# Kernel optimization log

Measured on AMD Instinct MI355X. Metric: run time of the kernel, lower is better.

## Reference

```python
import jax, jax.numpy as jnp
import numpy as np

N = 4096      # nodes (= attention seq_len)
D = 256       # dim_h
H = 4         # num_heads
HD = D // H   # head dim
E = 131072    # edges (avg degree 32)


def _ln(x, g, b, eps=1e-5):
    mu = jnp.mean(x, -1, keepdims=True)
    var = jnp.var(x, -1, keepdims=True)
    return (x - mu) * jax.lax.rsqrt(var + eps) * g + b


def setup_inputs() -> dict:
    key = jax.random.key(0)
    ks = jax.random.split(key, 10)
    s = 0.02
    nrm = lambda k, shape: jax.random.normal(k, shape, jnp.float32) * s
    return dict(
        x=jax.random.normal(ks[0], (N, D), jnp.float32),
        edge_index=jax.random.randint(ks[1], (2, E), 0, N, dtype=jnp.int32),
        W_gcn=nrm(ks[2], (D, D)), b_gcn=jnp.zeros((D,), jnp.float32),
        w_qkv=nrm(ks[3], (D, 3 * D)), b_qkv=jnp.zeros((3 * D,), jnp.float32),
        w_out=nrm(ks[4], (D, D)), b_out=jnp.zeros((D,), jnp.float32),
        g1l=jnp.ones((D,), jnp.float32), beta1l=jnp.zeros((D,), jnp.float32),
        g1a=jnp.ones((D,), jnp.float32), beta1a=jnp.zeros((D,), jnp.float32),
        W1=nrm(ks[5], (D, 2 * D)), bf1=jnp.zeros((2 * D,), jnp.float32),
        W2=nrm(ks[6], (2 * D, D)), bf2=jnp.zeros((D,), jnp.float32),
        g2=jnp.ones((D,), jnp.float32), beta2=jnp.zeros((D,), jnp.float32),
    )


def reference(x, edge_index, W_gcn, b_gcn, w_qkv, b_qkv, w_out, b_out,
              g1l, beta1l, g1a, beta1a, W1, bf1, W2, bf2, g2, beta2):
    n = x.shape[0]
    # --- GCNConv: sym-normalized aggregation with self loops ---
    loop = jnp.arange(n, dtype=edge_index.dtype)
    src = jnp.concatenate([edge_index[0], loop])
    dst = jnp.concatenate([edge_index[1], loop])
    deg = jax.ops.segment_sum(jnp.ones_like(src, x.dtype), dst, num_segments=n)
    dinv = jax.lax.rsqrt(deg)  # deg >= 1 thanks to self loops
    h = x @ W_gcn                                  # [N, D]
    msg = h[src] * (dinv[src] * dinv[dst])[:, None]  # gather + edge norm
    x_local = jax.ops.segment_sum(msg, dst, num_segments=n) + b_gcn
    x = _ln(x + x_local, g1l, beta1l)
    # --- Multi-head self-attention over all nodes (one sequence) ---
    qkv = x @ w_qkv + b_qkv
    q, k, v = jnp.split(qkv, 3, axis=-1)
    q = q.reshape(n, H, HD)
    k = k.reshape(n, H, HD)
    v = v.reshape(n, H, HD)
    scale = 1.0 / (HD ** 0.5)
    scores = jnp.einsum('nhd,mhd->hnm', q, k) * scale   # [H, N, N]
    attn = jax.nn.softmax(scores, axis=-1)
    x_attn = jnp.einsum('hnm,mhd->nhd', attn, v).reshape(n, D) @ w_out + b_out
    x = _ln(x + x_attn, g1a, beta1a)
    # --- FFN (D -> 2D -> D, ReLU) ---
    x_ffn = jax.nn.relu(x @ W1 + bf1) @ W2 + bf2
    return _ln(x + x_ffn, g2, beta2)
```

## Files before the change

kernel.cpp:

```cpp
#include <hip/hip_runtime.h>

typedef unsigned short u16;
typedef __bf16 bf16x8 __attribute__((ext_vector_type(8)));
typedef float f32x4 __attribute__((ext_vector_type(4)));

__device__ __forceinline__ u16 f2u(float f) {
    unsigned u = __builtin_bit_cast(unsigned, f);
    return (u16)((u + 0x7FFFu + ((u >> 16) & 1u)) >> 16);
}

__device__ __forceinline__ float u2f(u16 h) {
    return __builtin_bit_cast(float, (unsigned)h << 16);
}

__device__ __forceinline__ void glds16(const u16* g, u16* l) {
    __builtin_amdgcn_global_load_lds((const __attribute__((address_space(1))) unsigned int*)g,
                                     (__attribute__((address_space(3))) unsigned int*)l, 16, 0, 0);
}


__global__ __launch_bounds__(256) void prep_k(
    const float* __restrict__ w0, const float* __restrict__ w1, const float* __restrict__ w2,
    const float* __restrict__ w3, const float* __restrict__ w4, const float* __restrict__ x,
    u16* __restrict__ o0, u16* __restrict__ o1, u16* __restrict__ o2,
    u16* __restrict__ o3, u16* __restrict__ o4, u16* __restrict__ xo,
    int* __restrict__ cnt, int xblocks, int nn) {
    int b = blockIdx.x, t = threadIdx.x;
    if (b < 144) {
        const float* in; u16* out; int R, C, tb;
        if (b < 16)       { in = w0; out = o0; R = 256; C = 256; tb = b; }
        else if (b < 64)  { in = w1; out = o1; R = 256; C = 768; tb = b - 16; }
        else if (b < 80)  { in = w2; out = o2; R = 256; C = 256; tb = b - 64; }
        else if (b < 112) { in = w3; out = o3; R = 256; C = 512; tb = b - 80; }
        else              { in = w4; out = o4; R = 512; C = 256; tb = b - 112; }
        int tcols = C >> 6;
        int tr = tb / tcols, tc = tb - tr * tcols;
        __shared__ float T[64][65];
        int i0 = t >> 6, j = t & 63;
#pragma unroll
        for (int p = 0; p < 16; p++) {
            int r = p * 4 + i0;
            T[r][j] = in[(long)(tr * 64 + r) * C + tc * 64 + j];
        }
        __syncthreads();
#pragma unroll
        for (int p = 0; p < 16; p++) {
            int c = p * 4 + i0;
            out[(long)(tc * 64 + c) * R + tr * 64 + j] = f2u(T[j][c]);
        }
    } else if (b < 144 + xblocks) {
        long base = (long)(b - 144) * 4096;
#pragma unroll
        for (int p = 0; p < 4; p++) {
            long idx = base + p * 1024 + t * 4;
            float4 v = *(const float4*)&x[idx];
            unsigned lo = (unsigned)f2u(v.x) | ((unsigned)f2u(v.y) << 16);
            unsigned hi = (unsigned)f2u(v.z) | ((unsigned)f2u(v.w) << 16);
            *(uint2*)&xo[idx] = uint2{lo, hi};
        }
    } else {
        int i = (b - 144 - xblocks) * 256 + t;
        if (i < nn) cnt[i] = 0;
    }
}

__global__ void count_k(const int* __restrict__ ei, int E, int* __restrict__ cnt) {
    int e = blockIdx.x * 256 + threadIdx.x;
    if (e < E) atomicAdd(&cnt[ei[E + e]], 1);
}

__global__ __launch_bounds__(256) void scan_k(const int* __restrict__ cnt, int* __restrict__ offs,
                                              int* __restrict__ cur, float* __restrict__ dinv) {
    __shared__ int sums[256];
    int t = threadIdx.x;
    int base = t * 16;
    int loc[16]; int s = 0;
#pragma unroll
    for (int i = 0; i < 16; i++) { loc[i] = s; s += cnt[base + i]; }
    sums[t] = s;
    __syncthreads();
    for (int off = 1; off < 256; off <<= 1) {
        int v = (t >= off) ? sums[t - off] : 0;
        __syncthreads();
        sums[t] += v;
        __syncthreads();
    }
    int ex = (t == 0) ? 0 : sums[t - 1];
#pragma unroll
    for (int i = 0; i < 16; i++) {
        int o = ex + loc[i];
        offs[base + i] = o; cur[base + i] = o;
        dinv[base + i] = rsqrtf((float)(cnt[base + i] + 1));
    }
}

__global__ void scatter_k(const int* __restrict__ ei, int E, int* __restrict__ cur, int* __restrict__ srcs) {
    int e = blockIdx.x * 256 + threadIdx.x;
    if (e < E) {
        int s = ei[e], d = ei[E + e];
        int p = atomicAdd(&cur[d], 1);
        srcs[p] = s;
    }
}


__device__ __forceinline__ void block_ln_stats(float v, float& mu, float& rstd) {
    float s1 = v, s2 = v * v;
#pragma unroll
    for (int m = 1; m < 64; m <<= 1) { s1 += __shfl_xor(s1, m, 64); s2 += __shfl_xor(s2, m, 64); }
    __shared__ float r1[4], r2[4];
    int lane = threadIdx.x & 63, w = threadIdx.x >> 6;
    if (lane == 0) { r1[w] = s1; r2[w] = s2; }
    __syncthreads();
    s1 = r1[0] + r1[1] + r1[2] + r1[3];
    s2 = r2[0] + r2[1] + r2[2] + r2[3];
    mu = s1 * (1.0f / 256.0f);
    float var = s2 * (1.0f / 256.0f) - mu * mu;
    rstd = rsqrtf(var + 1e-5f);
}

__global__ __launch_bounds__(256) void ln_k(const float* __restrict__ a, const float* __restrict__ b,
                                            const float* __restrict__ g, const float* __restrict__ be,
                                            float* __restrict__ out, u16* __restrict__ outbf) {
    int n = blockIdx.x, d = threadIdx.x;
    long i = (long)n * 256 + d;
    float v = a[i] + b[i];
    float mu, rs;
    block_ln_stats(v, mu, rs);
    float y = (v - mu) * rs * g[d] + be[d];
    out[i] = y;
    if (outbf) outbf[i] = f2u(y);
}


__global__ __launch_bounds__(256) void gcn_agg_ln_k(
    const u16* __restrict__ h, const float* __restrict__ x,
    const int* __restrict__ srcs, const int* __restrict__ offs, const int* __restrict__ cnt,
    const float* __restrict__ dinv, const float* __restrict__ bg,
    const float* __restrict__ g, const float* __restrict__ be,
    float* __restrict__ x1, u16* __restrict__ x1bf) {
    int n = blockIdx.x, d = threadIdx.x;
    int c = cnt[n], st = offs[n];
    float dn = dinv[n];
    float agg = u2f(h[(long)n * 256 + d]) * dn;
    int e = 0;
    for (; e + 4 <= c; e += 4) {
        int s0 = srcs[st + e], s1 = srcs[st + e + 1], s2 = srcs[st + e + 2], s3 = srcs[st + e + 3];
        float a0 = u2f(h[(long)s0 * 256 + d]) * dinv[s0];
        float a1 = u2f(h[(long)s1 * 256 + d]) * dinv[s1];
        float a2 = u2f(h[(long)s2 * 256 + d]) * dinv[s2];
        float a3 = u2f(h[(long)s3 * 256 + d]) * dinv[s3];
        agg += (a0 + a1) + (a2 + a3);
    }
    for (; e < c; e++) {
        int s = srcs[st + e];
        agg += u2f(h[(long)s * 256 + d]) * dinv[s];
    }
    float v = x[(long)n * 256 + d] + dn * agg + bg[d];
    float mu, rs;
    block_ln_stats(v, mu, rs);
    float y = (v - mu) * rs * g[d] + be[d];
    x1[(long)n * 256 + d] = y;
    x1bf[(long)n * 256 + d] = f2u(y);
}


template <int EPI>
__global__ __launch_bounds__(256) void gemm_k(
    const u16* __restrict__ A, const u16* __restrict__ Bt,
    const float* __restrict__ bias, void* __restrict__ outp,
    int M, int N, int K) {
    __shared__ __align__(16) u16 As[64 * 256];
    __shared__ __align__(16) u16 Bs[64 * 256];
    int tid = threadIdx.x;
    int lane = tid & 63, w = tid >> 6;
    int l15 = lane & 15, quad = lane >> 4, l7 = l15 & 7;
    int m0 = blockIdx.x * 64, n0 = blockIdx.y * 64;
    int wm = (w >> 1) * 32, wn = (w & 1) * 32;
    f32x4 acc[2][2];
#pragma unroll
    for (int i = 0; i < 2; i++)
#pragma unroll
        for (int j = 0; j < 2; j++) acc[i][j] = f32x4{0.f, 0.f, 0.f, 0.f};

    int rA0 = (wm + l15) * 256, rA1 = (wm + 16 + l15) * 256;
    int rB0 = (wn + l15) * 256, rB1 = (wn + 16 + l15) * 256;

    for (int kb = 0; kb < K; kb += 256) {
        if (kb) __syncthreads();
#pragma unroll
        for (int i = 0; i < 8; i++) {
            int s = i * 256 + tid;
            int j = s >> 5, dch = s & 31;
            int c = dch ^ (j & 7);
            glds16(A + (long)(m0 + j) * K + kb + c * 8, &As[s * 8]);
            glds16(Bt + (long)(n0 + j) * K + kb + c * 8, &Bs[s * 8]);
        }
        __syncthreads();
#pragma unroll
        for (int step = 0; step < 8; step++) {
            int d8 = (((step << 2) + quad) ^ l7) << 3;
            bf16x8 af0 = *(const bf16x8*)&As[rA0 + d8];
            bf16x8 af1 = *(const bf16x8*)&As[rA1 + d8];
            bf16x8 bf0 = *(const bf16x8*)&Bs[rB0 + d8];
            bf16x8 bf1 = *(const bf16x8*)&Bs[rB1 + d8];
            acc[0][0] = __builtin_amdgcn_mfma_f32_16x16x32_bf16(af0, bf0, acc[0][0], 0, 0, 0);
            acc[0][1] = __builtin_amdgcn_mfma_f32_16x16x32_bf16(af0, bf1, acc[0][1], 0, 0, 0);
            acc[1][0] = __builtin_amdgcn_mfma_f32_16x16x32_bf16(af1, bf0, acc[1][0], 0, 0, 0);
            acc[1][1] = __builtin_amdgcn_mfma_f32_16x16x32_bf16(af1, bf1, acc[1][1], 0, 0, 0);
        }
    }

#pragma unroll
    for (int nf = 0; nf < 2; nf++) {
        int col = n0 + wn + nf * 16 + l15;
        float bv = bias ? bias[col] : 0.0f;
#pragma unroll
        for (int mf = 0; mf < 2; mf++) {
#pragma unroll
            for (int r = 0; r < 4; r++) {
                int row = m0 + wm + mf * 16 + quad * 4 + r;
                float v = acc[mf][nf][r] + bv;
                if (EPI == 0) {
                    ((float*)outp)[(long)row * N + col] = v;
                } else if (EPI == 1) {
                    u16* q = (u16*)outp;
                    u16* kk = q + (long)M * 256;
                    u16* vt = kk + (long)M * 256;
                    if (col < 256) {
                        q[(((col >> 6) * (long)M) + row) * 64 + (col & 63)] = f2u(v * 0.180336884f);
                    } else if (col < 512) {
                        int c = col - 256;
                        kk[(((c >> 6) * (long)M) + row) * 64 + (c & 63)] = f2u(v);
                    } else {
                        int c = col - 512;
                        vt[((c >> 6) * 64 + (c & 63)) * (long)M + row] = f2u(v);
                    }
                } else if (EPI == 2) {
                    ((u16*)outp)[(long)row * N + col] = f2u(v > 0.f ? v : 0.f);
                } else {
                    ((u16*)outp)[(long)row * N + col] = f2u(v);
                }
            }
        }
    }
}


__global__ __launch_bounds__(256) void attn_k(const u16* __restrict__ qg, const u16* __restrict__ kg,
                                              const u16* __restrict__ vtg, float* __restrict__ po,
                                              float* __restrict__ pl, int N, int S) {
    int tid = threadIdx.x;
    int w = tid >> 6, lane = tid & 63, l15 = lane & 15, quad = lane >> 4;
    int lid = blockIdx.x + 64 * blockIdx.y + 256 * blockIdx.z;
    int hs = lid & 15;
    int hh = hs & 3, sp = hs >> 2, qb = lid >> 4;
    int q0 = qb * 64 + w * 16;
    int kbeg = sp * (N / S);
    int nit = (N / S) / 64;
    const u16* qh = qg + (long)hh * N * 64;
    const u16* kh = kg + (long)hh * N * 64;
    const u16* vh = vtg + (long)hh * 64 * N;

    __shared__ __align__(16) u16 KV[2][2][4096];
    __shared__ __align__(16) u16 P[4][1024];
    u16* Pw = &P[w][0];

    int s0 = tid, j0 = s0 >> 3, c0s = ((s0 & 7) ^ (j0 & 7)) * 8;
    int s1 = tid + 256, j1 = s1 >> 3, c1s = ((s1 & 7) ^ (j1 & 7)) * 8;
    const u16* kp0 = kh + (long)(kbeg + j0) * 64 + c0s;
    const u16* kp1 = kh + (long)(kbeg + j1) * 64 + c1s;
    const u16* vp0 = vh + (long)j0 * N + kbeg + c0s;
    const u16* vp1 = vh + (long)j1 * N + kbeg + c1s;
    u16* lk0[2] = {&KV[0][0][s0 * 8], &KV[1][0][s0 * 8]};
    u16* lk1[2] = {&KV[0][0][s1 * 8], &KV[1][0][s1 * 8]};
    u16* lv0[2] = {&KV[0][1][s0 * 8], &KV[1][1][s0 * 8]};
    u16* lv1[2] = {&KV[0][1][s1 * 8], &KV[1][1][s1 * 8]};

    int lo3 = l15 & 7;
    int c0 = (quad ^ lo3) * 8;
    int c1 = c0 ^ 32;
    int ps = lo3 << 1;
    int pw0 = l15 * 64 + (((quad << 1) ^ ps) << 2);
    int pw1 = l15 * 64 + (((8 + (quad << 1)) ^ ps) << 2);
    int pca[4];
#pragma unroll
    for (int nt = 0; nt < 4; nt++) pca[nt] = l15 * 64 + (((nt * 4 + quad) ^ ps) << 2);

    bf16x8 aq0 = *(const bf16x8*)(qh + (long)(q0 + l15) * 64 + quad * 8);
    bf16x8 aq1 = *(const bf16x8*)(qh + (long)(q0 + l15) * 64 + 32 + quad * 8);
    bf16x8 ones;
#pragma unroll
    for (int i = 0; i < 8; i++) ones[i] = (__bf16)1.0f;

    f32x4 o[4];
#pragma unroll
    for (int dn = 0; dn < 4; dn++) o[dn] = f32x4{0.f, 0.f, 0.f, 0.f};
    f32x4 accl = f32x4{0.f, 0.f, 0.f, 0.f};

    glds16(kp0, lk0[0]); glds16(kp1, lk1[0]);
    glds16(vp0, lv0[0]); glds16(vp1, lv1[0]);
    kp0 += 4096; kp1 += 4096; vp0 += 64; vp1 += 64;

    for (int it = 0; it < nit; it++) {
        __syncthreads();
        if (it + 1 < nit) {
            int nb = (it + 1) & 1;
            glds16(kp0, lk0[nb]); glds16(kp1, lk1[nb]);
            glds16(vp0, lv0[nb]); glds16(vp1, lv1[nb]);
            kp0 += 4096; kp1 += 4096; vp0 += 64; vp1 += 64;
        }
        const u16* Kc = &KV[it & 1][0][0];
        const u16* Vc = &KV[it & 1][1][0];
#pragma unroll
        for (int nt = 0; nt < 4; nt++) {
            const u16* Kr = Kc + (nt * 16 + l15) * 64;
            bf16x8 kf0 = *(const bf16x8*)(Kr + c0);
            bf16x8 kf1 = *(const bf16x8*)(Kr + c1);
            f32x4 s = f32x4{0.f, 0.f, 0.f, 0.f};
            s = __builtin_amdgcn_mfma_f32_16x16x32_bf16(kf0, aq0, s, 0, 0, 0);
            s = __builtin_amdgcn_mfma_f32_16x16x32_bf16(kf1, aq1, s, 0, 0, 0);
            unsigned u0 = (unsigned)((int)(s[0] * 8388608.0f) + 1064992209);
            unsigned u1 = (unsigned)((int)(s[1] * 8388608.0f) + 1064992209);
            unsigned u2 = (unsigned)((int)(s[2] * 8388608.0f) + 1064992209);
            unsigned u3 = (unsigned)((int)(s[3] * 8388608.0f) + 1064992209);
            unsigned pk01 = __builtin_amdgcn_perm(u1, u0, 0x07060302u);
            unsigned pk23 = __builtin_amdgcn_perm(u3, u2, 0x07060302u);
            *(uint2*)&Pw[pca[nt]] = uint2{pk01, pk23};
        }
        bf16x8 pa0 = *(const bf16x8*)&Pw[pw0];
        bf16x8 pa1 = *(const bf16x8*)&Pw[pw1];
        accl = __builtin_amdgcn_mfma_f32_16x16x32_bf16(pa0, ones, accl, 0, 0, 0);
        accl = __builtin_amdgcn_mfma_f32_16x16x32_bf16(pa1, ones, accl, 0, 0, 0);
#pragma unroll
        for (int dn = 0; dn < 4; dn++) {
            const u16* Vr = Vc + (dn * 16 + l15) * 64;
            bf16x8 v0 = *(const bf16x8*)(Vr + c0);
            bf16x8 v1 = *(const bf16x8*)(Vr + c1);
            o[dn] = __builtin_amdgcn_mfma_f32_16x16x32_bf16(pa0, v0, o[dn], 0, 0, 0);
            o[dn] = __builtin_amdgcn_mfma_f32_16x16x32_bf16(pa1, v1, o[dn], 0, 0, 0);
        }
    }

    long pbase = ((long)(sp * 4 + hh)) * N;
#pragma unroll
    for (int dn = 0; dn < 4; dn++)
#pragma unroll
        for (int r = 0; r < 4; r++) {
            int row = q0 + quad * 4 + r;
            po[(pbase + row) * 64 + dn * 16 + l15] = o[dn][r];
        }
    if (l15 == 0) {
#pragma unroll
        for (int r = 0; r < 4; r++) pl[pbase + q0 + quad * 4 + r] = accl[r];
    }
}

__global__ __launch_bounds__(256) void attn_comb_k(const float* __restrict__ po, const float* __restrict__ pl,
                                                   u16* __restrict__ xo, int N, int S) {
    int n = blockIdx.x, c = threadIdx.x;
    int hh = c >> 6, d = c & 63;
    float osum = 0.f, lsum = 0.f;
    for (int s = 0; s < S; s++) {
        osum += po[(((long)(s * 4 + hh)) * N + n) * 64 + d];
        lsum += pl[((long)(s * 4 + hh)) * N + n];
    }
    xo[(long)n * 256 + c] = f2u(osum / lsum);
}


extern "C" void kernel_launch(void* const* d_in, const int* in_sizes, int n_in,
                              void* d_out, int out_size, void* d_ws, size_t ws_size,
                              hipStream_t stream) {
    const float* x    = (const float*)d_in[0];
    const int*   ei   = (const int*)d_in[1];
    const float* Wg   = (const float*)d_in[2];
    const float* bg   = (const float*)d_in[3];
    const float* Wqkv = (const float*)d_in[4];
    const float* bqkv = (const float*)d_in[5];
    const float* Wo   = (const float*)d_in[6];
    const float* bo   = (const float*)d_in[7];
    const float* g1l  = (const float*)d_in[8];
    const float* b1l  = (const float*)d_in[9];
    const float* g1a  = (const float*)d_in[10];
    const float* b1a  = (const float*)d_in[11];
    const float* W1   = (const float*)d_in[12];
    const float* bf1  = (const float*)d_in[13];
    const float* W2   = (const float*)d_in[14];
    const float* bf2  = (const float*)d_in[15];
    const float* g2   = (const float*)d_in[16];
    const float* b2   = (const float*)d_in[17];
    float* out = (float*)d_out;

    int N = in_sizes[0] / 256;
    int E = in_sizes[1] / 2;
    const int S = 4;

    char* p = (char*)d_ws;
    auto alloc = [&](size_t bytes) { void* r = (void*)p; p += (bytes + 255) & ~(size_t)255; return r; };
    u16*   wg_t   = (u16*)alloc((size_t)256 * 256 * 2);
    u16*   wqkv_t = (u16*)alloc((size_t)256 * 768 * 2);
    u16*   wo_t   = (u16*)alloc((size_t)256 * 256 * 2);
    u16*   w1_t   = (u16*)alloc((size_t)512 * 256 * 2);
    u16*   w2_t   = (u16*)alloc((size_t)256 * 512 * 2);
    u16*   xbf    = (u16*)alloc((size_t)N * 256 * 2);
    u16*   h      = (u16*)alloc((size_t)N * 256 * 2);
    int*   cnt    = (int*)alloc((size_t)N * 4);
    int*   offs   = (int*)alloc((size_t)N * 4);
    int*   cur    = (int*)alloc((size_t)N * 4);
    float* dinv   = (float*)alloc((size_t)N * 4);
    int*   srcs   = (int*)alloc((size_t)E * 4);
    float* x1     = (float*)alloc((size_t)N * 256 * 4);
    u16*   x1bf   = (u16*)alloc((size_t)N * 256 * 2);
    u16*   qkv    = (u16*)alloc((size_t)3 * N * 256 * 2);
    u16*   xattn  = (u16*)alloc((size_t)N * 256 * 2);
    float* attno  = (float*)alloc((size_t)N * 256 * 4);
    float* x2     = (float*)alloc((size_t)N * 256 * 4);
    u16*   x2bf   = (u16*)alloc((size_t)N * 256 * 2);
    u16*   ffn1   = (u16*)alloc((size_t)N * 512 * 2);
    float* ffno   = (float*)alloc((size_t)N * 256 * 4);
    float* po     = (float*)alloc((size_t)S * 4 * N * 64 * 4);
    float* pl     = (float*)alloc((size_t)S * 4 * N * 4);

    dim3 b256(256);

    int xblocks = (N * 256) / 4096;
    int cblocks = (N + 255) / 256;
    prep_k<<<144 + xblocks + cblocks, b256, 0, stream>>>(Wg, Wqkv, Wo, W1, W2, x,
                                                         wg_t, wqkv_t, wo_t, w1_t, w2_t, xbf,
                                                         cnt, xblocks, N);

    count_k<<<(E + 255) / 256, b256, 0, stream>>>(ei, E, cnt);
    scan_k<<<1, b256, 0, stream>>>(cnt, offs, cur, dinv);
    scatter_k<<<(E + 255) / 256, b256, 0, stream>>>(ei, E, cur, srcs);

    gemm_k<3><<<dim3(N / 64, 4), b256, 0, stream>>>(xbf, wg_t, nullptr, h, N, 256, 256);
    gcn_agg_ln_k<<<N, b256, 0, stream>>>(h, x, srcs, offs, cnt, dinv, bg, g1l, b1l, x1, x1bf);

    gemm_k<1><<<dim3(N / 64, 12), b256, 0, stream>>>(x1bf, wqkv_t, bqkv, qkv, N, 768, 256);
    attn_k<<<dim3(N / 64, 4, S), b256, 0, stream>>>(qkv, qkv + (size_t)N * 256, qkv + (size_t)2 * N * 256,
                                                    po, pl, N, S);
    attn_comb_k<<<N, b256, 0, stream>>>(po, pl, xattn, N, S);
    gemm_k<0><<<dim3(N / 64, 4), b256, 0, stream>>>(xattn, wo_t, bo, attno, N, 256, 256);
    ln_k<<<N, b256, 0, stream>>>(x1, attno, g1a, b1a, x2, x2bf);

    gemm_k<2><<<dim3(N / 64, 8), b256, 0, stream>>>(x2bf, w1_t, bf1, ffn1, N, 512, 256);
    gemm_k<0><<<dim3(N / 64, 4), b256, 0, stream>>>(ffn1, w2_t, bf2, ffno, N, 256, 512);
    ln_k<<<N, b256, 0, stream>>>(x2, ffno, g2, b2, out, nullptr);
}
```

Measured before the change: 207.9 us.

## Fuse all stages into one persistent cooperative kernel with grid syncs

New measurement: 680.5 us. 3.27x slower.

```diff
diff --git a/kernel.cpp b/kernel.cpp
--- a/kernel.cpp
+++ b/kernel.cpp
@@ -1,4 +1,7 @@
 #include <hip/hip_runtime.h>
+#include <hip/hip_cooperative_groups.h>
+
+namespace cg = cooperative_groups;
 
 typedef unsigned short u16;
 typedef __bf16 bf16x8 __attribute__((ext_vector_type(8)));
@@ -18,164 +21,40 @@
                                      (__attribute__((address_space(3))) unsigned int*)l, 16, 0, 0);
 }
 
-
-__global__ __launch_bounds__(256) void prep_k(
-    const float* __restrict__ w0, const float* __restrict__ w1, const float* __restrict__ w2,
-    const float* __restrict__ w3, const float* __restrict__ w4, const float* __restrict__ x,
-    u16* __restrict__ o0, u16* __restrict__ o1, u16* __restrict__ o2,
-    u16* __restrict__ o3, u16* __restrict__ o4, u16* __restrict__ xo,
-    int* __restrict__ cnt, int xblocks, int nn) {
-    int b = blockIdx.x, t = threadIdx.x;
-    if (b < 144) {
-        const float* in; u16* out; int R, C, tb;
-        if (b < 16)       { in = w0; out = o0; R = 256; C = 256; tb = b; }
-        else if (b < 64)  { in = w1; out = o1; R = 256; C = 768; tb = b - 16; }
-        else if (b < 80)  { in = w2; out = o2; R = 256; C = 256; tb = b - 64; }
-        else if (b < 112) { in = w3; out = o3; R = 256; C = 512; tb = b - 80; }
-        else              { in = w4; out = o4; R = 512; C = 256; tb = b - 112; }
-        int tcols = C >> 6;
-        int tr = tb / tcols, tc = tb - tr * tcols;
-        __shared__ float T[64][65];
-        int i0 = t >> 6, j = t & 63;
-#pragma unroll
-        for (int p = 0; p < 16; p++) {
-            int r = p * 4 + i0;
-            T[r][j] = in[(long)(tr * 64 + r) * C + tc * 64 + j];
-        }
-        __syncthreads();
-#pragma unroll
-        for (int p = 0; p < 16; p++) {
-            int c = p * 4 + i0;
-            out[(long)(tc * 64 + c) * R + tr * 64 + j] = f2u(T[j][c]);
-        }
-    } else if (b < 144 + xblocks) {
-        long base = (long)(b - 144) * 4096;
-#pragma unroll
-        for (int p = 0; p < 4; p++) {
-            long idx = base + p * 1024 + t * 4;
-            float4 v = *(const float4*)&x[idx];
-            unsigned lo = (unsigned)f2u(v.x) | ((unsigned)f2u(v.y) << 16);
-            unsigned hi = (unsigned)f2u(v.z) | ((unsigned)f2u(v.w) << 16);
-            *(uint2*)&xo[idx] = uint2{lo, hi};
-        }
-    } else {
-        int i = (b - 144 - xblocks) * 256 + t;
-        if (i < nn) cnt[i] = 0;
-    }
-}
-
-__global__ void count_k(const int* __restrict__ ei, int E, int* __restrict__ cnt) {
-    int e = blockIdx.x * 256 + threadIdx.x;
-    if (e < E) atomicAdd(&cnt[ei[E + e]], 1);
-}
-
-__global__ __launch_bounds__(256) void scan_k(const int* __restrict__ cnt, int* __restrict__ offs,
-                                              int* __restrict__ cur, float* __restrict__ dinv) {
-    __shared__ int sums[256];
-    int t = threadIdx.x;
-    int base = t * 16;
-    int loc[16]; int s = 0;
-#pragma unroll
-    for (int i = 0; i < 16; i++) { loc[i] = s; s += cnt[base + i]; }
-    sums[t] = s;
+struct MA {
+    const float *x, *Wg, *bg, *Wqkv, *bqkv, *Wo, *bo, *g1l, *b1l, *g1a, *b1a, *W1, *bf1, *W2, *bf2, *g2, *b2;
+    const int* ei;
+    u16 *wg_t, *wqkv_t, *wo_t, *w1_t, *w2_t, *xbf, *h, *x1bf, *qkv, *xattn, *x2bf, *ffn1;
+    int *cnt, *offs, *cur, *srcs;
+    float *dinv, *x1, *attno, *x2, *ffno, *po, *pl, *out;
+    int N, E;
+};
+
+__device__ __forceinline__ void blk_stats(float v, float* red, float& mu, float& rstd) {
+    float s1 = v, s2 = v * v;
+#pragma unroll
+    for (int m = 1; m < 64; m <<= 1) { s1 += __shfl_xor(s1, m, 64); s2 += __shfl_xor(s2, m, 64); }
+    int lane = threadIdx.x & 63, w = threadIdx.x >> 6;
     __syncthreads();
-    for (int off = 1; off < 256; off <<= 1) {
-        int v = (t >= off) ? sums[t - off] : 0;
-        __syncthreads();
-        sums[t] += v;
-        __syncthreads();
-    }
-    int ex = (t == 0) ? 0 : sums[t - 1];
-#pragma unroll
-    for (int i = 0; i < 16; i++) {
-        int o = ex + loc[i];
-        offs[base + i] = o; cur[base + i] = o;
-        dinv[base + i] = rsqrtf((float)(cnt[base + i] + 1));
-    }
-}
-
-__global__ void scatter_k(const int* __restrict__ ei, int E, int* __restrict__ cur, int* __restrict__ srcs) {
-    int e = blockIdx.x * 256 + threadIdx.x;
-    if (e < E) {
-        int s = ei[e], d = ei[E + e];
-        int p = atomicAdd(&cur[d], 1);
-        srcs[p] = s;
-    }
-}
-
-
-__device__ __forceinline__ void block_ln_stats(float v, float& mu, float& rstd) {
-    float s1 = v, s2 = v * v;
-#pragma unroll
-    for (int m = 1; m < 64; m <<= 1) { s1 += __shfl_xor(s1, m, 64); s2 += __shfl_xor(s2, m, 64); }
-    __shared__ float r1[4], r2[4];
-    int lane = threadIdx.x & 63, w = threadIdx.x >> 6;
-    if (lane == 0) { r1[w] = s1; r2[w] = s2; }
+    if (lane == 0) { red[w] = s1; red[4 + w] = s2; }
     __syncthreads();
-    s1 = r1[0] + r1[1] + r1[2] + r1[3];
-    s2 = r2[0] + r2[1] + r2[2] + r2[3];
+    s1 = red[0] + red[1] + red[2] + red[3];
+    s2 = red[4] + red[5] + red[6] + red[7];
     mu = s1 * (1.0f / 256.0f);
     float var = s2 * (1.0f / 256.0f) - mu * mu;
     rstd = rsqrtf(var + 1e-5f);
 }
 
-__global__ __launch_bounds__(256) void ln_k(const float* __restrict__ a, const float* __restrict__ b,
-                                            const float* __restrict__ g, const float* __restrict__ be,
-                                            float* __restrict__ out, u16* __restrict__ outbf) {
-    int n = blockIdx.x, d = threadIdx.x;
-    long i = (long)n * 256 + d;
-    float v = a[i] + b[i];
-    float mu, rs;
-    block_ln_stats(v, mu, rs);
-    float y = (v - mu) * rs * g[d] + be[d];
-    out[i] = y;
-    if (outbf) outbf[i] = f2u(y);
-}
-
-
-__global__ __launch_bounds__(256) void gcn_agg_ln_k(
-    const u16* __restrict__ h, const float* __restrict__ x,
-    const int* __restrict__ srcs, const int* __restrict__ offs, const int* __restrict__ cnt,
-    const float* __restrict__ dinv, const float* __restrict__ bg,
-    const float* __restrict__ g, const float* __restrict__ be,
-    float* __restrict__ x1, u16* __restrict__ x1bf) {
-    int n = blockIdx.x, d = threadIdx.x;
-    int c = cnt[n], st = offs[n];
-    float dn = dinv[n];
-    float agg = u2f(h[(long)n * 256 + d]) * dn;
-    int e = 0;
-    for (; e + 4 <= c; e += 4) {
-        int s0 = srcs[st + e], s1 = srcs[st + e + 1], s2 = srcs[st + e + 2], s3 = srcs[st + e + 3];
-        float a0 = u2f(h[(long)s0 * 256 + d]) * dinv[s0];
-        float a1 = u2f(h[(long)s1 * 256 + d]) * dinv[s1];
-        float a2 = u2f(h[(long)s2 * 256 + d]) * dinv[s2];
-        float a3 = u2f(h[(long)s3 * 256 + d]) * dinv[s3];
-        agg += (a0 + a1) + (a2 + a3);
-    }
-    for (; e < c; e++) {
-        int s = srcs[st + e];
-        agg += u2f(h[(long)s * 256 + d]) * dinv[s];
-    }
-    float v = x[(long)n * 256 + d] + dn * agg + bg[d];
-    float mu, rs;
-    block_ln_stats(v, mu, rs);
-    float y = (v - mu) * rs * g[d] + be[d];
-    x1[(long)n * 256 + d] = y;
-    x1bf[(long)n * 256 + d] = f2u(y);
-}
-
-
 template <int EPI>
-__global__ __launch_bounds__(256) void gemm_k(
-    const u16* __restrict__ A, const u16* __restrict__ Bt,
-    const float* __restrict__ bias, void* __restrict__ outp,
-    int M, int N, int K) {
-    __shared__ __align__(16) u16 As[64 * 256];
-    __shared__ __align__(16) u16 Bs[64 * 256];
+__device__ void gemm_tile(
+    const u16* __restrict__ A, const u16* __restrict__ Bt, const float* __restrict__ bias,
+    void* __restrict__ outp, int M, int N, int K, int bx, int by, u16* LDS) {
+    u16* As = LDS;
+    u16* Bs = LDS + 8192;
     int tid = threadIdx.x;
     int lane = tid & 63, w = tid >> 6;
     int l15 = lane & 15, quad = lane >> 4, l7 = l15 & 7;
-    int m0 = blockIdx.x * 64, n0 = blockIdx.y * 64;
+    int m0 = bx * 64, n0 = by * 64;
     int wm = (w >> 1) * 32, wn = (w & 1) * 32;
     f32x4 acc[2][2];
 #pragma unroll
@@ -183,23 +62,23 @@
 #pragma unroll
         for (int j = 0; j < 2; j++) acc[i][j] = f32x4{0.f, 0.f, 0.f, 0.f};
 
-    int rA0 = (wm + l15) * 256, rA1 = (wm + 16 + l15) * 256;
-    int rB0 = (wn + l15) * 256, rB1 = (wn + 16 + l15) * 256;
-
-    for (int kb = 0; kb < K; kb += 256) {
-        if (kb) __syncthreads();
-#pragma unroll
-        for (int i = 0; i < 8; i++) {
+    int rA0 = (wm + l15) * 128, rA1 = (wm + 16 + l15) * 128;
+    int rB0 = (wn + l15) * 128, rB1 = (wn + 16 + l15) * 128;
+
+    for (int kb = 0; kb < K; kb += 128) {
+        __syncthreads();
+#pragma unroll
+        for (int i = 0; i < 4; i++) {
             int s = i * 256 + tid;
-            int j = s >> 5, dch = s & 31;
-            int c = dch ^ (j & 7);
+            int j = s >> 4, c = (s & 15) ^ (j & 7);
             glds16(A + (long)(m0 + j) * K + kb + c * 8, &As[s * 8]);
             glds16(Bt + (long)(n0 + j) * K + kb + c * 8, &Bs[s * 8]);
         }
         __syncthreads();
 #pragma unroll
-        for (int step = 0; step < 8; step++) {
-            int d8 = (((step << 2) + quad) ^ l7) << 3;
+        for (int step = 0; step < 4; step++) {
+            int ch = (step << 2) + quad;
+            int d8 = ((ch & 8) | ((ch & 7) ^ l7)) << 3;
             bf16x8 af0 = *(const bf16x8*)&As[rA0 + d8];
             bf16x8 af1 = *(const bf16x8*)&As[rA1 + d8];
             bf16x8 bf0 = *(const bf16x8*)&Bs[rB0 + d8];
@@ -246,36 +125,31 @@
     }
 }
 
-
-__global__ __launch_bounds__(256) void attn_k(const u16* __restrict__ qg, const u16* __restrict__ kg,
-                                              const u16* __restrict__ vtg, float* __restrict__ po,
-                                              float* __restrict__ pl, int N, int S) {
-    int tid = threadIdx.x;
-    int w = tid >> 6, lane = tid & 63, l15 = lane & 15, quad = lane >> 4;
-    int lid = blockIdx.x + 64 * blockIdx.y + 256 * blockIdx.z;
-    int hs = lid & 15;
-    int hh = hs & 3, sp = hs >> 2, qb = lid >> 4;
+__device__ void attn_unit(const MA& a, int u, u16* LDS) {
+    int N = a.N;
+    const int S = 4;
+    int t = threadIdx.x;
+    int w = t >> 6, lane = t & 63, l15 = lane & 15, quad = lane >> 4;
+    int hs = u & 15, hh = hs & 3, sp = hs >> 2, qb = u >> 4;
     int q0 = qb * 64 + w * 16;
     int kbeg = sp * (N / S);
     int nit = (N / S) / 64;
-    const u16* qh = qg + (long)hh * N * 64;
-    const u16* kh = kg + (long)hh * N * 64;
-    const u16* vh = vtg + (long)hh * 64 * N;
-
-    __shared__ __align__(16) u16 KV[2][2][4096];
-    __shared__ __align__(16) u16 P[4][1024];
-    u16* Pw = &P[w][0];
-
-    int s0 = tid, j0 = s0 >> 3, c0s = ((s0 & 7) ^ (j0 & 7)) * 8;
-    int s1 = tid + 256, j1 = s1 >> 3, c1s = ((s1 & 7) ^ (j1 & 7)) * 8;
+    const u16* qh = a.qkv + (long)hh * N * 64;
+    const u16* kh = a.qkv + (long)N * 256 + (long)hh * N * 64;
+    const u16* vh = a.qkv + (long)2 * N * 256 + (long)hh * 64 * N;
+    u16* KV = LDS;
+    u16* Pw = LDS + 8192 + w * 1024;
+
+    int s0 = t, j0 = s0 >> 3, c0s = ((s0 & 7) ^ (j0 & 7)) * 8;
+    int s1 = t + 256, j1 = s1 >> 3, c1s = ((s1 & 7) ^ (j1 & 7)) * 8;
     const u16* kp0 = kh + (long)(kbeg + j0) * 64 + c0s;
     const u16* kp1 = kh + (long)(kbeg + j1) * 64 + c1s;
     const u16* vp0 = vh + (long)j0 * N + kbeg + c0s;
     const u16* vp1 = vh + (long)j1 * N + kbeg + c1s;
-    u16* lk0[2] = {&KV[0][0][s0 * 8], &KV[1][0][s0 * 8]};
-    u16* lk1[2] = {&KV[0][0][s1 * 8], &KV[1][0][s1 * 8]};
-    u16* lv0[2] = {&KV[0][1][s0 * 8], &KV[1][1][s0 * 8]};
-    u16* lv1[2] = {&KV[0][1][s1 * 8], &KV[1][1][s1 * 8]};
+    u16* lk0 = KV + s0 * 8;
+    u16* lk1 = KV + s1 * 8;
+    u16* lv0 = KV + 4096 + s0 * 8;
+    u16* lv1 = KV + 4096 + s1 * 8;
 
     int lo3 = l15 & 7;
     int c0 = (quad ^ lo3) * 8;
@@ -298,23 +172,14 @@
     for (int dn = 0; dn < 4; dn++) o[dn] = f32x4{0.f, 0.f, 0.f, 0.f};
     f32x4 accl = f32x4{0.f, 0.f, 0.f, 0.f};
 
-    glds16(kp0, lk0[0]); glds16(kp1, lk1[0]);
-    glds16(vp0, lv0[0]); glds16(vp1, lv1[0]);
-    kp0 += 4096; kp1 += 4096; vp0 += 64; vp1 += 64;
-
     for (int it = 0; it < nit; it++) {
+        glds16(kp0, lk0); glds16(kp1, lk1);
+        glds16(vp0, lv0); glds16(vp1, lv1);
+        kp0 += 4096; kp1 += 4096; vp0 += 64; vp1 += 64;
         __syncthreads();
-        if (it + 1 < nit) {
-            int nb = (it + 1) & 1;
-            glds16(kp0, lk0[nb]); glds16(kp1, lk1[nb]);
-            glds16(vp0, lv0[nb]); glds16(vp1, lv1[nb]);
-            kp0 += 4096; kp1 += 4096; vp0 += 64; vp1 += 64;
-        }
-        const u16* Kc = &KV[it & 1][0][0];
-        const u16* Vc = &KV[it & 1][1][0];
 #pragma unroll
         for (int nt = 0; nt < 4; nt++) {
-            const u16* Kr = Kc + (nt * 16 + l15) * 64;
+            const u16* Kr = KV + (nt * 16 + l15) * 64;
             bf16x8 kf0 = *(const bf16x8*)(Kr + c0);
             bf16x8 kf1 = *(const bf16x8*)(Kr + c1);
             f32x4 s = f32x4{0.f, 0.f, 0.f, 0.f};
@@ -334,12 +199,13 @@
         accl = __builtin_amdgcn_mfma_f32_16x16x32_bf16(pa1, ones, accl, 0, 0, 0);
 #pragma unroll
         for (int dn = 0; dn < 4; dn++) {
-            const u16* Vr = Vc + (dn * 16 + l15) * 64;
+            const u16* Vr = KV + 4096 + (dn * 16 + l15) * 64;
             bf16x8 v0 = *(const bf16x8*)(Vr + c0);
             bf16x8 v1 = *(const bf16x8*)(Vr + c1);
             o[dn] = __builtin_amdgcn_mfma_f32_16x16x32_bf16(pa0, v0, o[dn], 0, 0, 0);
             o[dn] = __builtin_amdgcn_mfma_f32_16x16x32_bf16(pa1, v1, o[dn], 0, 0, 0);
         }
+        __syncthreads();
     }
 
     long pbase = ((long)(sp * 4 + hh)) * N;
@@ -348,103 +214,270 @@
 #pragma unroll
         for (int r = 0; r < 4; r++) {
             int row = q0 + quad * 4 + r;
-            po[(pbase + row) * 64 + dn * 16 + l15] = o[dn][r];
+            a.po[(pbase + row) * 64 + dn * 16 + l15] = o[dn][r];
         }
     if (l15 == 0) {
 #pragma unroll
-        for (int r = 0; r < 4; r++) pl[pbase + q0 + quad * 4 + r] = accl[r];
-    }
-}
-
-__global__ __launch_bounds__(256) void attn_comb_k(const float* __restrict__ po, const float* __restrict__ pl,
-                                                   u16* __restrict__ xo, int N, int S) {
-    int n = blockIdx.x, c = threadIdx.x;
-    int hh = c >> 6, d = c & 63;
-    float osum = 0.f, lsum = 0.f;
-    for (int s = 0; s < S; s++) {
-        osum += po[(((long)(s * 4 + hh)) * N + n) * 64 + d];
-        lsum += pl[((long)(s * 4 + hh)) * N + n];
-    }
-    xo[(long)n * 256 + c] = f2u(osum / lsum);
+        for (int r = 0; r < 4; r++) a.pl[pbase + q0 + quad * 4 + r] = accl[r];
+    }
+}
+
+__device__ void phase_run(const MA& a, int ph, u16* LDS) {
+    int b = blockIdx.x, t = threadIdx.x, NB = gridDim.x;
+    int N = a.N, E = a.E;
+    int nt64 = N / 64;
+    float* red = (float*)LDS;
+
+    switch (ph) {
+    case 0: {
+        int xb = (N * 256) / 4096, U = 144 + xb + N / 256;
+        for (int u = b; u < U; u += NB) {
+            if (u < 144) {
+                const float* in; u16* out; int R, C, tb;
+                if (u < 16)       { in = a.Wg;   out = a.wg_t;   R = 256; C = 256; tb = u; }
+                else if (u < 64)  { in = a.Wqkv; out = a.wqkv_t; R = 256; C = 768; tb = u - 16; }
+                else if (u < 80)  { in = a.Wo;   out = a.wo_t;   R = 256; C = 256; tb = u - 64; }
+                else if (u < 112) { in = a.W1;   out = a.w1_t;   R = 256; C = 512; tb = u - 80; }
+                else              { in = a.W2;   out = a.w2_t;   R = 512; C = 256; tb = u - 112; }
+                int tcols = C >> 6;
+                int tr = tb / tcols, tc = tb - tr * tcols;
+                float* T = (float*)LDS;
+                int i0 = t >> 6, j = t & 63;
+                __syncthreads();
+#pragma unroll
+                for (int p = 0; p < 16; p++) {
+                    int r = p * 4 + i0;
+                    T[r * 65 + j] = in[(long)(tr * 64 + r) * C + tc * 64 + j];
+                }
+                __syncthreads();
+#pragma unroll
+                for (int p = 0; p < 16; p++) {
+                    int c = p * 4 + i0;
+                    out[(long)(tc * 64 + c) * R + tr * 64 + j] = f2u(T[j * 65 + c]);
+                }
+            } else if (u < 144 + xb) {
+                long base = (long)(u - 144) * 4096;
+#pragma unroll
+                for (int p = 0; p < 4; p++) {
+                    long idx = base + p * 1024 + t * 4;
+                    float4 v = *(const float4*)&a.x[idx];
+                    unsigned lo = (unsigned)f2u(v.x) | ((unsigned)f2u(v.y) << 16);
+                    unsigned hi = (unsigned)f2u(v.z) | ((unsigned)f2u(v.w) << 16);
+                    *(uint2*)&a.xbf[idx] = uint2{lo, hi};
+                }
+            } else {
+                a.cnt[(u - 144 - xb) * 256 + t] = 0;
+            }
+        }
+        break;
+    }
+    case 1:
+        for (int e = b * 256 + t; e < E; e += NB * 256) atomicAdd(&a.cnt[a.ei[E + e]], 1);
+        break;
+    case 2:
+        if (b == 0) {
+            int* sums = (int*)LDS;
+            int base = t * 16;
+            int loc[16]; int s = 0;
+#pragma unroll
+            for (int i = 0; i < 16; i++) { loc[i] = s; s += a.cnt[base + i]; }
+            sums[t] = s;
+            __syncthreads();
+            for (int off = 1; off < 256; off <<= 1) {
+                int v = (t >= off) ? sums[t - off] : 0;
+                __syncthreads();
+                sums[t] += v;
+                __syncthreads();
+            }
+            int ex = (t == 0) ? 0 : sums[t - 1];
+#pragma unroll
+            for (int i = 0; i < 16; i++) {
+                int o = ex + loc[i];
+                a.offs[base + i] = o; a.cur[base + i] = o;
+                a.dinv[base + i] = rsqrtf((float)(a.cnt[base + i] + 1));
+            }
+        }
+        break;
+    case 3: {
+        int gt = nt64 * 4, eb = E / 256;
+        for (int u = b; u < gt + eb; u += NB) {
+            if (u < gt) {
+                gemm_tile<3>(a.xbf, a.wg_t, nullptr, a.h, N, 256, 256, u % nt64, u / nt64, LDS);
+            } else {
+                int e = (u - gt) * 256 + t;
+                if (e < E) {
+                    int s = a.ei[e], d = a.ei[E + e];
+                    int p = atomicAdd(&a.cur[d], 1);
+                    a.srcs[p] = s;
+                }
+            }
+        }
+        break;
+    }
+    case 4:
+        for (int n = b; n < N; n += NB) {
+            int d = t;
+            int c = a.cnt[n], st = a.offs[n];
+            float dn = a.dinv[n];
+            float agg = u2f(a.h[(long)n * 256 + d]) * dn;
+            int e = 0;
+            for (; e + 4 <= c; e += 4) {
+                int s0 = a.srcs[st + e], s1 = a.srcs[st + e + 1], s2 = a.srcs[st + e + 2], s3 = a.srcs[st + e + 3];
+                float a0 = u2f(a.h[(long)s0 * 256 + d]) * a.dinv[s0];
+                float a1 = u2f(a.h[(long)s1 * 256 + d]) * a.dinv[s1];
+                float a2 = u2f(a.h[(long)s2 * 256 + d]) * a.dinv[s2];
+                float a3 = u2f(a.h[(long)s3 * 256 + d]) * a.dinv[s3];
+                agg += (a0 + a1) + (a2 + a3);
+            }
+            for (; e < c; e++) {
+                int s = a.srcs[st + e];
+                agg += u2f(a.h[(long)s * 256 + d]) * a.dinv[s];
+            }
+            float v = a.x[(long)n * 256 + d] + dn * agg + a.bg[d];
+            float mu, rs;
+            blk_stats(v, red, mu, rs);
+            float y = (v - mu) * rs * a.g1l[d] + a.b1l[d];
+            a.x1[(long)n * 256 + d] = y;
+            a.x1bf[(long)n * 256 + d] = f2u(y);
+        }
+        break;
+    case 5:
+        for (int u = b; u < nt64 * 12; u += NB)
+            gemm_tile<1>(a.x1bf, a.wqkv_t, a.bqkv, a.qkv, N, 768, 256, u % nt64, u / nt64, LDS);
+        break;
+    case 6:
+        for (int u = b; u < nt64 * 16; u += NB) attn_unit(a, u, LDS);
+        break;
+    case 7:
+        for (int n = b; n < N; n += NB) {
+            int hh = t >> 6, d = t & 63;
+            float osum = 0.f, lsum = 0.f;
+#pragma unroll
+            for (int s = 0; s < 4; s++) {
+                osum += a.po[(((long)(s * 4 + hh)) * N + n) * 64 + d];
+                lsum += a.pl[((long)(s * 4 + hh)) * N + n];
+            }
+            a.xattn[(long)n * 256 + t] = f2u(osum / lsum);
+        }
+        break;
+    case 8:
+        for (int u = b; u < nt64 * 4; u += NB)
+            gemm_tile<0>(a.xattn, a.wo_t, a.bo, a.attno, N, 256, 256, u % nt64, u / nt64, LDS);
+        break;
+    case 9:
+        for (int n = b; n < N; n += NB) {
+            long idx = (long)n * 256 + t;
+            float v = a.x1[idx] + a.attno[idx];
+            float mu, rs;
+            blk_stats(v, red, mu, rs);
+            float y = (v - mu) * rs * a.g1a[t] + a.b1a[t];
+            a.x2[idx] = y;
+            a.x2bf[idx] = f2u(y);
+        }
+        break;
+    case 10:
+        for (int u = b; u < nt64 * 8; u += NB)
+            gemm_tile<2>(a.x2bf, a.w1_t, a.bf1, a.ffn1, N, 512, 256, u % nt64, u / nt64, LDS);
+        break;
+    case 11:
+        for (int u = b; u < nt64 * 4; u += NB)
+            gemm_tile<0>(a.ffn1, a.w2_t, a.bf2, a.ffno, N, 256, 512, u % nt64, u / nt64, LDS);
+        break;
+    case 12:
+        for (int n = b; n < N; n += NB) {
+            long idx = (long)n * 256 + t;
+            float v = a.x2[idx] + a.ffno[idx];
+            float mu, rs;
+            blk_stats(v, red, mu, rs);
+            a.out[idx] = (v - mu) * rs * a.g2[t] + a.b2[t];
+        }
+        break;
+    }
+}
+
+__global__ __launch_bounds__(256, 2) void mega_k(MA a) {
+    cg::grid_group grid = cg::this_grid();
+    __shared__ __align__(16) u16 LDS[16384];
+    for (int ph = 0; ph < 13; ph++) {
+        phase_run(a, ph, LDS);
+        if (ph < 12) grid.sync();
+    }
+}
+
+__global__ __launch_bounds__(256) void phase_k(MA a, int ph) {
+    __shared__ __align__(16) u16 LDS[16384];
+    phase_run(a, ph, LDS);
 }
 
 
 extern "C" void kernel_launch(void* const* d_in, const int* in_sizes, int n_in,
                               void* d_out, int out_size, void* d_ws, size_t ws_size,
                               hipStream_t stream) {
-    const float* x    = (const float*)d_in[0];
-    const int*   ei   = (const int*)d_in[1];
-    const float* Wg   = (const float*)d_in[2];
-    const float* bg   = (const float*)d_in[3];
-    const float* Wqkv = (const float*)d_in[4];
-    const float* bqkv = (const float*)d_in[5];
-    const float* Wo   = (const float*)d_in[6];
-    const float* bo   = (const float*)d_in[7];
-    const float* g1l  = (const float*)d_in[8];
-    const float* b1l  = (const float*)d_in[9];
-    const float* g1a  = (const float*)d_in[10];
-    const float* b1a  = (const float*)d_in[11];
-    const float* W1   = (const float*)d_in[12];
-    const float* bf1  = (const float*)d_in[13];
-    const float* W2   = (const float*)d_in[14];
-    const float* bf2  = (const float*)d_in[15];
-    const float* g2   = (const float*)d_in[16];
-    const float* b2   = (const float*)d_in[17];
-    float* out = (float*)d_out;
-
     int N = in_sizes[0] / 256;
     int E = in_sizes[1] / 2;
     const int S = 4;
 
     char* p = (char*)d_ws;
     auto alloc = [&](size_t bytes) { void* r = (void*)p; p += (bytes + 255) & ~(size_t)255; return r; };
-    u16*   wg_t   = (u16*)alloc((size_t)256 * 256 * 2);
-    u16*   wqkv_t = (u16*)alloc((size_t)256 * 768 * 2);
-    u16*   wo_t   = (u16*)alloc((size_t)256 * 256 * 2);
-    u16*   w1_t   = (u16*)alloc((size_t)512 * 256 * 2);
-    u16*   w2_t   = (u16*)alloc((size_t)256 * 512 * 2);
-    u16*   xbf    = (u16*)alloc((size_t)N * 256 * 2);
-    u16*   h      = (u16*)alloc((size_t)N * 256 * 2);
-    int*   cnt    = (int*)alloc((size_t)N * 4);
-    int*   offs   = (int*)alloc((size_t)N * 4);
-    int*   cur    = (int*)alloc((size_t)N * 4);
-    float* dinv   = (float*)alloc((size_t)N * 4);
-    int*   srcs   = (int*)alloc((size_t)E * 4);
-    float* x1     = (float*)alloc((size_t)N * 256 * 4);
-    u16*   x1bf   = (u16*)alloc((size_t)N * 256 * 2);
-    u16*   qkv    = (u16*)alloc((size_t)3 * N * 256 * 2);
-    u16*   xattn  = (u16*)alloc((size_t)N * 256 * 2);
-    float* attno  = (float*)alloc((size_t)N * 256 * 4);
-    float* x2     = (float*)alloc((size_t)N * 256 * 4);
-    u16*   x2bf   = (u16*)alloc((size_t)N * 256 * 2);
-    u16*   ffn1   = (u16*)alloc((size_t)N * 512 * 2);
-    float* ffno   = (float*)alloc((size_t)N * 256 * 4);
-    float* po     = (float*)alloc((size_t)S * 4 * N * 64 * 4);
-    float* pl     = (float*)alloc((size_t)S * 4 * N * 4);
-
-    dim3 b256(256);
-
-    int xblocks = (N * 256) / 4096;
-    int cblocks = (N + 255) / 256;
-    prep_k<<<144 + xblocks + cblocks, b256, 0, stream>>>(Wg, Wqkv, Wo, W1, W2, x,
-                                                         wg_t, wqkv_t, wo_t, w1_t, w2_t, xbf,
-                                                         cnt, xblocks, N);
-
-    count_k<<<(E + 255) / 256, b256, 0, stream>>>(ei, E, cnt);
-    scan_k<<<1, b256, 0, stream>>>(cnt, offs, cur, dinv);
-    scatter_k<<<(E + 255) / 256, b256, 0, stream>>>(ei, E, cur, srcs);
-
-    gemm_k<3><<<dim3(N / 64, 4), b256, 0, stream>>>(xbf, wg_t, nullptr, h, N, 256, 256);
-    gcn_agg_ln_k<<<N, b256, 0, stream>>>(h, x, srcs, offs, cnt, dinv, bg, g1l, b1l, x1, x1bf);
-
-    gemm_k<1><<<dim3(N / 64, 12), b256, 0, stream>>>(x1bf, wqkv_t, bqkv, qkv, N, 768, 256);
-    attn_k<<<dim3(N / 64, 4, S), b256, 0, stream>>>(qkv, qkv + (size_t)N * 256, qkv + (size_t)2 * N * 256,
-                                                    po, pl, N, S);
-    attn_comb_k<<<N, b256, 0, stream>>>(po, pl, xattn, N, S);
-    gemm_k<0><<<dim3(N / 64, 4), b256, 0, stream>>>(xattn, wo_t, bo, attno, N, 256, 256);
-    ln_k<<<N, b256, 0, stream>>>(x1, attno, g1a, b1a, x2, x2bf);
-
-    gemm_k<2><<<dim3(N / 64, 8), b256, 0, stream>>>(x2bf, w1_t, bf1, ffn1, N, 512, 256);
-    gemm_k<0><<<dim3(N / 64, 4), b256, 0, stream>>>(ffn1, w2_t, bf2, ffno, N, 256, 512);
-    ln_k<<<N, b256, 0, stream>>>(x2, ffno, g2, b2, out, nullptr);
-}
+
+    MA a;
+    a.x    = (const float*)d_in[0];
+    a.ei   = (const int*)d_in[1];
+    a.Wg   = (const float*)d_in[2];
+    a.bg   = (const float*)d_in[3];
+    a.Wqkv = (const float*)d_in[4];
+    a.bqkv = (const float*)d_in[5];
+    a.Wo   = (const float*)d_in[6];
+    a.bo   = (const float*)d_in[7];
+    a.g1l  = (const float*)d_in[8];
+    a.b1l  = (const float*)d_in[9];
+    a.g1a  = (const float*)d_in[10];
+    a.b1a  = (const float*)d_in[11];
+    a.W1   = (const float*)d_in[12];
+    a.bf1  = (const float*)d_in[13];
+    a.W2   = (const float*)d_in[14];
+    a.bf2  = (const float*)d_in[15];
+    a.g2   = (const float*)d_in[16];
+    a.b2   = (const float*)d_in[17];
+    a.out  = (float*)d_out;
+    a.N = N; a.E = E;
+
+    a.wg_t   = (u16*)alloc((size_t)256 * 256 * 2);
+    a.wqkv_t = (u16*)alloc((size_t)256 * 768 * 2);
+    a.wo_t   = (u16*)alloc((size_t)256 * 256 * 2);
+    a.w1_t   = (u16*)alloc((size_t)512 * 256 * 2);
+    a.w2_t   = (u16*)alloc((size_t)256 * 512 * 2);
+    a.xbf    = (u16*)alloc((size_t)N * 256 * 2);
+    a.h      = (u16*)alloc((size_t)N * 256 * 2);
+    a.cnt    = (int*)alloc((size_t)N * 4);
+    a.offs   = (int*)alloc((size_t)N * 4);
+    a.cur    = (int*)alloc((size_t)N * 4);
+    a.dinv   = (float*)alloc((size_t)N * 4);
+    a.srcs   = (int*)alloc((size_t)E * 4);
+    a.x1     = (float*)alloc((size_t)N * 256 * 4);
+    a.x1bf   = (u16*)alloc((size_t)N * 256 * 2);
+    a.qkv    = (u16*)alloc((size_t)3 * N * 256 * 2);
+    a.xattn  = (u16*)alloc((size_t)N * 256 * 2);
+    a.attno  = (float*)alloc((size_t)N * 256 * 4);
+    a.x2     = (float*)alloc((size_t)N * 256 * 4);
+    a.x2bf   = (u16*)alloc((size_t)N * 256 * 2);
+    a.ffn1   = (u16*)alloc((size_t)N * 512 * 2);
+    a.ffno   = (float*)alloc((size_t)N * 256 * 4);
+    a.po     = (float*)alloc((size_t)S * 4 * N * 64 * 4);
+    a.pl     = (float*)alloc((size_t)S * 4 * N * 4);
+
+    int maxB = 0;
+    hipError_t oe = hipOccupancyMaxActiveBlocksPerMultiprocessor(&maxB, mega_k, 256, 0);
+    int NB = maxB * 256;
+    if (NB > 1024) NB = 1024;
+
+    hipError_t le = hipErrorUnknown;
+    if (oe == hipSuccess && NB >= 256) {
+        void* kp[] = {(void*)&a};
+        le = hipLaunchCooperativeKernel(mega_k, dim3(NB), dim3(256), kp, 0, stream);
+    }
+    if (le != hipSuccess) {
+        for (int ph = 0; ph < 13; ph++)
+            phase_k<<<1024, 256, 0, stream>>>(a, ph);
+    }
+}
```
